# Performance work log

Measured on AMD Instinct MI355X. Metric: run time of the kernel, lower is better.

Reference implementation:

```python
import jax, jax.numpy as jnp
import numpy as np

B, T, C, E, K, CAP, H = 8, 2048, 1024, 8, 2, 4096, 4096


def setup_inputs() -> dict:
    key = jax.random.key(0)
    ks = jax.random.split(key, 6)
    s = 0.02
    return {
        "x": jax.random.normal(ks[0], (B, T, C), jnp.float32),
        "rw1": s * jax.random.normal(ks[1], (C, H), jnp.float32),
        "rb1": jnp.zeros((H,), jnp.float32),
        "rw2": s * jax.random.normal(ks[2], (H, E), jnp.float32),
        "rb2": jnp.zeros((E,), jnp.float32),
        "ew1": s * jax.random.normal(ks[3], (E, C, H), jnp.float32),
        "eb1": jnp.zeros((E, H), jnp.float32),
        "ew2": s * jax.random.normal(ks[4], (E, H, C), jnp.float32),
        "eb2": jnp.zeros((E, C), jnp.float32),
    }


def reference(x, rw1, rb1, rw2, rb2, ew1, eb1, ew2, eb2):
    Bx, Tx, Cx = x.shape
    N = Bx * Tx
    # Router FFN -> gating logits [B,T,E]
    logits = jax.nn.relu(x @ rw1 + rb1) @ rw2 + rb2
    vals, ids = jax.lax.top_k(logits, K)           # [B,T,K]
    probs = jax.nn.softmax(vals, axis=-1)          # [B,T,K]

    ids_f = ids.reshape(N * K)                     # expert id per (token, k) slot
    probs_f = probs.reshape(N * K)
    xr = jnp.repeat(x.reshape(N, Cx), K, axis=0)   # [N*K, C], token order preserved

    # position of each slot within its expert's capacity buffer
    m = jax.nn.one_hot(ids_f, E, dtype=jnp.int32)  # [N*K, E]
    pos = jnp.cumsum(m, axis=0) - 1
    pos_tok = jnp.take_along_axis(pos, ids_f[:, None], axis=1)[:, 0]
    keep = (pos_tok < CAP).astype(x.dtype)         # drop tokens over capacity (padding)
    pos_c = jnp.clip(pos_tok, 0, CAP - 1)

    # dispatch: scatter tokens into per-expert padded buffers [E, CAP, C]
    disp = jnp.zeros((E, CAP, Cx), x.dtype).at[ids_f, pos_c].add(xr * keep[:, None])

    # expert FFN, batched over experts
    h = jax.nn.relu(jnp.einsum('enc,ech->enh', disp, ew1) + eb1[:, None, :])
    eo = jnp.einsum('enh,ehc->enc', h, ew2) + eb2[:, None, :]

    # combine: gather expert outputs back, weight by gate prob, sum over k
    y = eo[ids_f, pos_c] * (probs_f * keep)[:, None]   # [N*K, C]
    return y.reshape(Bx, Tx, K, Cx).sum(axis=2)
```

## Files before the change

kernel.cpp:

```cpp
#include <hip/hip_runtime.h>
#include <cstdint>
#include <type_traits>

#define B_    8
#define T_    2048
#define C_    1024
#define E_    8
#define K_    2
#define CAP_  4096
#define H_    4096
#define NTOK  (B_ * T_)
#define NSLOT (NTOK * K_)
#define KR_   3072
#define MARGIN_ 8e-3f

typedef __bf16    bf16x8 __attribute__((ext_vector_type(8)));
typedef _Float16  half8  __attribute__((ext_vector_type(8)));
typedef float     f32x4  __attribute__((ext_vector_type(4)));

#define AS1 __attribute__((address_space(1)))
#define AS3 __attribute__((address_space(3)))

static __device__ __forceinline__ float b2f(unsigned short u) {
    union { float f; unsigned int i; } v; v.i = ((unsigned int)u) << 16; return v.f;
}
static __device__ __forceinline__ unsigned short f2b(float f) {
    unsigned int x = __float_as_uint(f);
    unsigned int r = (x + 0x7fffu + ((x >> 16) & 1u)) >> 16;
    return (unsigned short)r;
}
static __device__ __forceinline__ unsigned short f2h(float f) {
    _Float16 h = (_Float16)f;
    return __builtin_bit_cast(unsigned short, h);
}

template<int W> static __device__ __forceinline__ void vm_wait() {
    if constexpr (W == 4) asm volatile("s_waitcnt vmcnt(4)" ::: "memory");
    else if constexpr (W == 0) asm volatile("s_waitcnt vmcnt(0)" ::: "memory");
}

template<int RELU, typename TC, bool F16, bool SCAT>
__global__ __launch_bounds__(512, 2) void gemm256_8ph(
    const unsigned short* __restrict__ A, const unsigned short* __restrict__ BT,
    const float* __restrict__ bias, TC* __restrict__ Cout,
    int Kd, int Nld, int NT,
    long sA, long sB, long sBias, long sC,
    const int* __restrict__ lst, const int* __restrict__ cnt)
{
    extern __shared__ char smem[];

    const int z = blockIdx.z;
    A    += (size_t)z * sA;
    BT   += (size_t)z * sB;
    bias += (size_t)z * sBias;
    Cout += (size_t)z * sC;

    const int gx = gridDim.x;
    const int nwg = gx * gridDim.y;
    int wg = blockIdx.y * gx + blockIdx.x;
    wg = (wg & 7) * (nwg >> 3) + (wg >> 3);
    const int bm = (wg / gx) * 256;
    const int bn = (wg % gx) * 256;

    int nf = 0;
    if constexpr (SCAT) {
        nf = *cnt;
        if (bm >= nf) return;
    }

    const int tid  = threadIdx.x;
    const int lane = tid & 63;
    const int wid  = tid >> 6;
    const int wrow = (wid >> 2) * 128;
    const int wcol = (wid & 3) * 64;
    const int fr = lane & 15;
    const int fq = lane >> 4;

    const size_t rbA = (size_t)Kd * 2;
    const char* Ag = (const char*)A  + (size_t)bm * rbA;
    const char* Bg = (const char*)BT + (size_t)bn * rbA;

    f32x4 acc[8][4];
#pragma unroll
    for (int i = 0; i < 8; i++)
#pragma unroll
        for (int j = 0; j < 4; j++) acc[i][j] = (f32x4){0.f, 0.f, 0.f, 0.f};

    auto STAGE_A = [&](int kt) {
        char* d = smem + (size_t)(kt & 1) * 65536;
        const size_t kb = (size_t)kt * 128;
#pragma unroll
        for (int r = 0; r < 4; ++r) {
            const int o    = r * 8192 + tid * 16;
            const int row  = o >> 7;
            const int slot = (o >> 4) & 7;
            const int ss   = (slot ^ (row & 7)) << 4;
            __builtin_amdgcn_global_load_lds(
                (const AS1 void*)(Ag + (size_t)row * rbA + kb + ss),
                (AS3 void*)(d + r * 8192 + wid * 1024), 16, 0, 0);
        }
    };
    auto STAGE_B = [&](int kt) {
        char* d = smem + (size_t)(kt & 1) * 65536 + 32768;
        const size_t kb = (size_t)kt * 128;
#pragma unroll
        for (int r = 0; r < 4; ++r) {
            const int o    = r * 8192 + tid * 16;
            const int row  = o >> 7;
            const int slot = (o >> 4) & 7;
            const int ss   = (slot ^ (row & 7)) << 4;
            __builtin_amdgcn_global_load_lds(
                (const AS1 void*)(Bg + (size_t)row * rbA + kb + ss),
                (AS3 void*)(d + r * 8192 + wid * 1024), 16, 0, 0);
        }
    };

    auto LDA = [&](int kt, int mi, int kk) -> bf16x8 {
        const char* base = smem + (size_t)(kt & 1) * 65536;
        const int row  = wrow + mi * 16 + fr;
        const int slot = (kk * 4 + fq) ^ (row & 7);
        return *(const bf16x8*)(base + row * 128 + slot * 16);
    };
    auto LDB = [&](int kt, int ni, int kk) -> bf16x8 {
        const char* base = smem + (size_t)(kt & 1) * 65536 + 32768;
        const int row  = wcol + ni * 16 + fr;
        const int slot = (kk * 4 + fq) ^ (row & 7);
        return *(const bf16x8*)(base + row * 128 + slot * 16);
    };
    auto MFMA = [&](f32x4 c, bf16x8 a, bf16x8 b) -> f32x4 {
        if constexpr (F16)
            return __builtin_amdgcn_mfma_f32_16x16x32_f16(
                __builtin_bit_cast(half8, a), __builtin_bit_cast(half8, b), c, 0, 0, 0);
        else
            return __builtin_amdgcn_mfma_f32_16x16x32_bf16(a, b, c, 0, 0, 0);
    };

    STAGE_A(0); STAGE_B(0); STAGE_B(1);
    vm_wait<4>();
    __builtin_amdgcn_s_barrier();

    bf16x8 a[4], bb[4];
    for (int kt = 0; kt < NT; ++kt) {
#pragma unroll
        for (int i = 0; i < 4; ++i) a[i]  = LDA(kt, i, 0);
#pragma unroll
        for (int i = 0; i < 4; ++i) bb[i] = LDB(kt, i, 0);
        if (kt + 1 < NT) STAGE_A(kt + 1);
        __builtin_amdgcn_s_barrier();
        __builtin_amdgcn_s_setprio(1);
#pragma unroll
        for (int mi = 0; mi < 4; ++mi)
#pragma unroll
            for (int ni = 0; ni < 4; ++ni)
                acc[mi][ni] = MFMA(acc[mi][ni], a[mi], bb[ni]);
        __builtin_amdgcn_s_setprio(0);
        __builtin_amdgcn_s_barrier();
#pragma unroll
        for (int i = 0; i < 4; ++i) a[i] = LDA(kt, 4 + i, 0);
        __builtin_amdgcn_s_barrier();
        __builtin_amdgcn_s_setprio(1);
#pragma unroll
        for (int mi = 0; mi < 4; ++mi)
#pragma unroll
            for (int ni = 0; ni < 4; ++ni)
                acc[4 + mi][ni] = MFMA(acc[4 + mi][ni], a[mi], bb[ni]);
        __builtin_amdgcn_s_setprio(0);
        __builtin_amdgcn_s_barrier();
#pragma unroll
        for (int i = 0; i < 4; ++i) a[i]  = LDA(kt, i, 1);
#pragma unroll
        for (int i = 0; i < 4; ++i) bb[i] = LDB(kt, i, 1);
        __builtin_amdgcn_s_barrier();
        __builtin_amdgcn_s_setprio(1);
#pragma unroll
        for (int mi = 0; mi < 4; ++mi)
#pragma unroll
            for (int ni = 0; ni < 4; ++ni)
                acc[mi][ni] = MFMA(acc[mi][ni], a[mi], bb[ni]);
        __builtin_amdgcn_s_setprio(0);
        __builtin_amdgcn_s_barrier();
#pragma unroll
        for (int i = 0; i < 4; ++i) a[i] = LDA(kt, 4 + i, 1);
        if (kt + 2 < NT) STAGE_B(kt + 2);
        if (kt + 1 < NT) {
            if (kt + 2 < NT) vm_wait<4>();
            else             vm_wait<0>();
        }
        __builtin_amdgcn_s_barrier();
        __builtin_amdgcn_s_setprio(1);
#pragma unroll
        for (int mi = 0; mi < 4; ++mi)
#pragma unroll
            for (int ni = 0; ni < 4; ++ni)
                acc[4 + mi][ni] = MFMA(acc[4 + mi][ni], a[mi], bb[ni]);
        __builtin_amdgcn_s_setprio(0);
        __builtin_amdgcn_s_barrier();
    }

    const float* bias_o = bias;
    asm volatile("" : "+s"(bias_o));
#pragma unroll
    for (int mi = 0; mi < 8; ++mi) {
#pragma unroll
        for (int ni = 0; ni < 4; ++ni) {
            const int c = bn + wcol + ni * 16 + fr;
            const float bv = bias_o[c];
#pragma unroll
            for (int rg = 0; rg < 4; ++rg) {
                const int r = bm + wrow + mi * 16 + fq * 4 + rg;
                float v = acc[mi][ni][rg] + bv;
                if (RELU) v = fmaxf(v, 0.f);
                if constexpr (SCAT) {
                    if (r < nf) {
                        const int t = lst[r];
                        ((float*)Cout)[(size_t)t * Nld + c] = v;
                    }
                } else if constexpr (std::is_same_v<TC, float>) {
                    Cout[(size_t)r * Nld + c] = v;
                } else {
                    Cout[(size_t)r * Nld + c] = f2b(v);
                }
            }
        }
    }
}

__global__ __launch_bounds__(256) void split_x16(
    const float* __restrict__ x, unsigned short* __restrict__ x16)
{
    const int n = blockIdx.x;
    const int c = threadIdx.x * 4;
    const float4 v = *(const float4*)(x + (size_t)n * C_ + c);
    ushort4 u;
    u.x = f2h(v.x); u.y = f2h(v.y); u.z = f2h(v.z); u.w = f2h(v.w);
    *(ushort4*)(x16 + (size_t)n * C_ + c) = u;
}

__global__ __launch_bounds__(256) void gather_split(
    const float* __restrict__ x, const int* __restrict__ list,
    const int* __restrict__ count, unsigned short* __restrict__ Axc)
{
    const int i = blockIdx.x;
    if (i >= *count) return;
    const int n = list[i];
    const int c = threadIdx.x * 4;
    const float4 v = *(const float4*)(x + (size_t)n * C_ + c);
    ushort4 hi, lo;
    hi.x = f2b(v.x); lo.x = f2b(v.x - b2f(hi.x));
    hi.y = f2b(v.y); lo.y = f2b(v.y - b2f(hi.y));
    hi.z = f2b(v.z); lo.z = f2b(v.z - b2f(hi.z));
    hi.w = f2b(v.w); lo.w = f2b(v.w - b2f(hi.w));
    unsigned short* row = Axc + (size_t)i * KR_;
    *(ushort4*)(row + c)          = hi;
    *(ushort4*)(row + C_ + c)     = lo;
    *(ushort4*)(row + 2 * C_ + c) = hi;
}

__global__ __launch_bounds__(256) void split_w(
    const float* __restrict__ in, unsigned short* __restrict__ out)
{
    __shared__ float t[32][33];
    const int rb = blockIdx.y * 32;
    const int cb = blockIdx.x * 32;
    const int tr = threadIdx.x >> 3, tc = (threadIdx.x & 7) * 4;
    const float4 v = *(const float4*)(in + (size_t)(rb + tr) * H_ + cb + tc);
    t[tr][tc + 0] = v.x; t[tr][tc + 1] = v.y; t[tr][tc + 2] = v.z; t[tr][tc + 3] = v.w;
    __syncthreads();
    ushort4 hi, lo;
    float f;
    f = t[tc + 0][tr]; hi.x = f2b(f); lo.x = f2b(f - b2f(hi.x));
    f = t[tc + 1][tr]; hi.y = f2b(f); lo.y = f2b(f - b2f(hi.y));
    f = t[tc + 2][tr]; hi.z = f2b(f); lo.z = f2b(f - b2f(hi.z));
    f = t[tc + 3][tr]; hi.w = f2b(f); lo.w = f2b(f - b2f(hi.w));
    unsigned short* row = out + (size_t)(cb + tr) * KR_;
    *(ushort4*)(row + rb + tc)           = hi;
    *(ushort4*)(row + C_ + rb + tc)      = hi;
    *(ushort4*)(row + 2 * C_ + rb + tc)  = lo;
}

template<bool H16>
__global__ __launch_bounds__(256) void transpose_cvt(
    const float* __restrict__ in, unsigned short* __restrict__ out, int R, int Ncols)
{
    __shared__ float t[32][33];
    const size_t zoff = (size_t)blockIdx.z * R * Ncols;
    in  += zoff;
    out += zoff;
    const int rb = blockIdx.y * 32, cb = blockIdx.x * 32;
    const int tr = threadIdx.x >> 3, tc = (threadIdx.x & 7) * 4;
    const float4 v = *(const float4*)(in + (size_t)(rb + tr) * Ncols + cb + tc);
    t[tr][tc + 0] = v.x; t[tr][tc + 1] = v.y; t[tr][tc + 2] = v.z; t[tr][tc + 3] = v.w;
    __syncthreads();
    ushort4 u;
    if constexpr (H16) {
        u.x = f2h(t[tc + 0][tr]); u.y = f2h(t[tc + 1][tr]);
        u.z = f2h(t[tc + 2][tr]); u.w = f2h(t[tc + 3][tr]);
    } else {
        u.x = f2b(t[tc + 0][tr]); u.y = f2b(t[tc + 1][tr]);
        u.z = f2b(t[tc + 2][tr]); u.w = f2b(t[tc + 3][tr]);
    }
    *(ushort4*)(out + (size_t)(cb + tr) * R + rb + tc) = u;
}

template<int MODE>
__global__ __launch_bounds__(256) void router_topk_m(
    const float* __restrict__ h1, const float* __restrict__ rw2,
    const float* __restrict__ rb2, int* __restrict__ ids, float* __restrict__ probs,
    int* __restrict__ flagv, int* __restrict__ list, int* __restrict__ count)
{
    const int n = blockIdx.x;
    if (MODE == 1 && !flagv[n]) return;
    const float* hrow = h1 + (size_t)n * H_;
    float acc[E_];
#pragma unroll
    for (int e = 0; e < E_; e++) acc[e] = 0.f;
    for (int h = threadIdx.x; h < H_; h += 256) {
        const float hv = hrow[h];
        const float4 w0 = *(const float4*)(rw2 + (size_t)h * E_);
        const float4 w1 = *(const float4*)(rw2 + (size_t)h * E_ + 4);
        acc[0] = fmaf(hv, w0.x, acc[0]); acc[1] = fmaf(hv, w0.y, acc[1]);
        acc[2] = fmaf(hv, w0.z, acc[2]); acc[3] = fmaf(hv, w0.w, acc[3]);
        acc[4] = fmaf(hv, w1.x, acc[4]); acc[5] = fmaf(hv, w1.y, acc[5]);
        acc[6] = fmaf(hv, w1.z, acc[6]); acc[7] = fmaf(hv, w1.w, acc[7]);
    }
    __shared__ float red[E_][256];
#pragma unroll
    for (int e = 0; e < E_; e++) red[e][threadIdx.x] = acc[e];
    __syncthreads();
    for (int st = 128; st > 0; st >>= 1) {
        if (threadIdx.x < st) {
#pragma unroll
            for (int e = 0; e < E_; e++) red[e][threadIdx.x] += red[e][threadIdx.x + st];
        }
        __syncthreads();
    }
    if (threadIdx.x == 0) {
        float v1 = -1e30f, v2 = -1e30f, v3 = -1e30f; int i1 = 0, i2 = 0;
#pragma unroll
        for (int e = 0; e < E_; e++) {
            const float v = red[e][0] + rb2[e];
            if (v > v1)      { v3 = v2; v2 = v1; i2 = i1; v1 = v; i1 = e; }
            else if (v > v2) { v3 = v2; v2 = v;  i2 = e; }
            else if (v > v3) { v3 = v; }
        }
        const float e2 = expf(v2 - v1);
        const float inv = 1.f / (1.f + e2);
        ids[n * 2] = i1;  ids[n * 2 + 1] = i2;
        probs[n * 2] = inv; probs[n * 2 + 1] = e2 * inv;
        if (MODE == 0) {
            if ((v1 - v2 < MARGIN_) || (v2 - v3 < MARGIN_)) {
                flagv[n] = 1;
                const int idx = atomicAdd(count, 1);
                list[idx] = n;
            }
        }
    }
}

__global__ __launch_bounds__(256) void compute_pos(
    const int* __restrict__ ids, int* __restrict__ pos)
{
    __shared__ int hist[256][E_];
    const int t = threadIdx.x;
    const int per = NSLOT / 256;
    int cnt[E_];
#pragma unroll
    for (int e = 0; e < E_; e++) cnt[e] = 0;
    const int s0 = t * per;
    for (int i = 0; i < per; i++) cnt[ids[s0 + i]]++;
#pragma unroll
    for (int e = 0; e < E_; e++) hist[t][e] = cnt[e];
    __syncthreads();
    if (t < E_) {
        int run = 0;
        for (int i = 0; i < 256; i++) { const int c = hist[i][t]; hist[i][t] = run; run += c; }
    }
    __syncthreads();
    int run[E_];
#pragma unroll
    for (int e = 0; e < E_; e++) run[e] = hist[t][e];
    for (int i = 0; i < per; i++) { const int e = ids[s0 + i]; pos[s0 + i] = run[e]++; }
}

__global__ __launch_bounds__(256) void dispatch_k(
    const float* __restrict__ x, const int* __restrict__ ids,
    const int* __restrict__ pos, unsigned short* __restrict__ disp)
{
    const int s = blockIdx.x;
    const int e = ids[s], p = pos[s];
    if (p >= CAP_) return;
    const int n = s >> 1;
    const float4 v = *(const float4*)(x + (size_t)n * C_ + threadIdx.x * 4);
    ushort4 u;
    u.x = f2b(v.x); u.y = f2b(v.y); u.z = f2b(v.z); u.w = f2b(v.w);
    *(ushort4*)(disp + ((size_t)e * CAP_ + p) * C_ + threadIdx.x * 4) = u;
}

__global__ __launch_bounds__(256) void combine_k(
    const unsigned short* __restrict__ eo, const int* __restrict__ ids,
    const int* __restrict__ pos, const float* __restrict__ probs,
    float* __restrict__ y)
{
    const int n = blockIdx.x;
    const int c = threadIdx.x * 4;
    float r0 = 0.f, r1 = 0.f, r2 = 0.f, r3 = 0.f;
#pragma unroll
    for (int k = 0; k < K_; k++) {
        const int p = pos[2 * n + k];
        if (p >= CAP_) continue;
        const int e = ids[2 * n + k];
        const float w = probs[2 * n + k];
        const ushort4 u = *(const ushort4*)(eo + ((size_t)e * CAP_ + p) * C_ + c);
        r0 = fmaf(w, b2f(u.x), r0); r1 = fmaf(w, b2f(u.y), r1);
        r2 = fmaf(w, b2f(u.z), r2); r3 = fmaf(w, b2f(u.w), r3);
    }
    *(float4*)(y + (size_t)n * C_ + c) = make_float4(r0, r1, r2, r3);
}

extern "C" void kernel_launch(void* const* d_in, const int* in_sizes, int n_in,
                              void* d_out, int out_size, void* d_ws, size_t ws_size,
                              hipStream_t stream)
{
    const float* x   = (const float*)d_in[0];
    const float* rw1 = (const float*)d_in[1];
    const float* rb1 = (const float*)d_in[2];
    const float* rw2 = (const float*)d_in[3];
    const float* rb2 = (const float*)d_in[4];
    const float* ew1 = (const float*)d_in[5];
    const float* eb1 = (const float*)d_in[6];
    const float* ew2 = (const float*)d_in[7];
    const float* eb2 = (const float*)d_in[8];
    float* y = (float*)d_out;

    char* ws = (char*)d_ws;
    float*          h1    = (float*)ws;
    unsigned short* hexp  = (unsigned short*)ws;
    unsigned short* W16T  = (unsigned short*)(ws + 268435456L);
    unsigned short* Axc   = (unsigned short*)(ws + 268435456L);
    unsigned short* disp  = (unsigned short*)(ws + 268435456L);
    unsigned short* eo    = (unsigned short*)(ws + 268435456L);
    unsigned short* BTW   = (unsigned short*)(ws + 335544320L);
    unsigned short* B2    = (unsigned short*)(ws + 369098752L);
    unsigned short* x16   = (unsigned short*)(ws + 369098752L);
    int*            ids   = (int*)  (ws + 402653184L);
    float*          probs = (float*)(ws + 402784256L);
    int*            pos   = (int*)  (ws + 402915328L);
    int*            flagv = (int*)  (ws + 403046400L);
    int*            list  = (int*)  (ws + 403111936L);
    int*            count = (int*)  (ws + 403177472L);

    const size_t LDSB = 131072;

    hipMemsetAsync(count, 0, 128, stream);
    hipMemsetAsync(flagv, 0, NTOK * sizeof(int), stream);

    split_x16<<<NTOK, 256, 0, stream>>>(x, x16);
    {
        dim3 g(H_ / 32, C_ / 32, 1);
        transpose_cvt<true><<<g, 256, 0, stream>>>(rw1, W16T, C_, H_);
    }
    {
        dim3 g(H_ / 256, NTOK / 256, 1);
        gemm256_8ph<1, float, true, false><<<g, 512, LDSB, stream>>>(
            x16, W16T, rb1, h1, C_, H_, C_ / 64, 0, 0, 0, 0, nullptr, nullptr);
    }
    router_topk_m<0><<<NTOK, 256, 0, stream>>>(h1, rw2, rb2, ids, probs,
                                               flagv, list, count);
    gather_split<<<NTOK, 256, 0, stream>>>(x, list, count, Axc);
    {
        dim3 g(H_ / 32, C_ / 32, 1);
        split_w<<<g, 256, 0, stream>>>(rw1, B2);
    }
    {
        dim3 g(H_ / 256, NTOK / 256, 1);
        gemm256_8ph<1, float, false, true><<<g, 512, LDSB, stream>>>(
            Axc, B2, rb1, h1, KR_, H_, KR_ / 64, 0, 0, 0, 0, list, count);
    }
    router_topk_m<1><<<NTOK, 256, 0, stream>>>(h1, rw2, rb2, ids, probs,
                                               flagv, list, count);
    compute_pos<<<1, 256, 0, stream>>>(ids, pos);
    dispatch_k<<<NSLOT, 256, 0, stream>>>(x, ids, pos, disp);
    {
        dim3 g(H_ / 32, C_ / 32, E_);
        transpose_cvt<false><<<g, 256, 0, stream>>>(ew1, BTW, C_, H_);
    }
    {
        dim3 g(H_ / 256, CAP_ / 256, E_);
        gemm256_8ph<1, unsigned short, false, false><<<g, 512, LDSB, stream>>>(
            disp, BTW, eb1, hexp, C_, H_, C_ / 64,
            (long)CAP_ * C_, (long)H_ * C_, (long)H_, (long)CAP_ * H_,
            nullptr, nullptr);
    }
    {
        dim3 g(C_ / 32, H_ / 32, E_);
        transpose_cvt<false><<<g, 256, 0, stream>>>(ew2, BTW, H_, C_);
    }
    {
        dim3 g(C_ / 256, CAP_ / 256, E_);
        gemm256_8ph<0, unsigned short, false, false><<<g, 512, LDSB, stream>>>(
            hexp, BTW, eb2, eo, H_, C_, H_ / 64,
            (long)CAP_ * H_, (long)C_ * H_, (long)C_, (long)CAP_ * C_,
            nullptr, nullptr);
    }
    combine_k<<<NTOK, 256, 0, stream>>>(eo, ids, pos, probs, y);
}
```

Before: 1.208 ms.

## Store router hidden in bf16, fix flagged tokens densely, fuse combine into expert GEMM

The first router GEMM now writes its hidden activations as bf16 instead of fp32, and the top-k kernel reads that bf16 buffer. The near-tie margin is widened so more tokens are recomputed in higher precision; their hidden rows go to a compact buffer indexed by list position instead of being scattered. The separate combine kernel is removed. The second expert GEMM epilogue now atomically adds prob-weighted outputs into y through a slot_of map, which y and slot_of memsets set up. This saves the h1 fp32 traffic and the eo round trip, but adds atomics, a larger fix-up set, and order-dependent float sums.

```diff
diff --git a/kernel.cpp b/kernel.cpp
--- a/kernel.cpp
+++ b/kernel.cpp
@@ -12,7 +12,8 @@
 #define NTOK  (B_ * T_)
 #define NSLOT (NTOK * K_)
 #define KR_   3072
-#define MARGIN_ 8e-3f
+#define MARGIN_ 3e-2f
+#define FIXCAP 8192
 
 typedef __bf16    bf16x8 __attribute__((ext_vector_type(8)));
 typedef _Float16  half8  __attribute__((ext_vector_type(8)));
@@ -39,13 +40,14 @@
     else if constexpr (W == 0) asm volatile("s_waitcnt vmcnt(0)" ::: "memory");
 }
 
-template<int RELU, typename TC, bool F16, bool SCAT>
+template<int RELU, typename TC, bool F16, int EPI>
 __global__ __launch_bounds__(512, 2) void gemm256_8ph(
     const unsigned short* __restrict__ A, const unsigned short* __restrict__ BT,
     const float* __restrict__ bias, TC* __restrict__ Cout,
     int Kd, int Nld, int NT,
     long sA, long sB, long sBias, long sC,
-    const int* __restrict__ lst, const int* __restrict__ cnt)
+    const int* __restrict__ cnt, const int* __restrict__ slotof,
+    const float* __restrict__ probsv, float* __restrict__ yout)
 {
     extern __shared__ char smem[];
 
@@ -63,7 +65,7 @@
     const int bn = (wg % gx) * 256;
 
     int nf = 0;
-    if constexpr (SCAT) {
+    if constexpr (EPI == 1) {
         nf = *cnt;
         if (bm >= nf) return;
     }
@@ -210,11 +212,13 @@
                 const int r = bm + wrow + mi * 16 + fq * 4 + rg;
                 float v = acc[mi][ni][rg] + bv;
                 if (RELU) v = fmaxf(v, 0.f);
-                if constexpr (SCAT) {
-                    if (r < nf) {
-                        const int t = lst[r];
-                        ((float*)Cout)[(size_t)t * Nld + c] = v;
-                    }
+                if constexpr (EPI == 1) {
+                    if (r < nf)
+                        ((float*)Cout)[(size_t)r * Nld + c] = v;
+                } else if constexpr (EPI == 2) {
+                    const int s = slotof[z * CAP_ + r];
+                    if (s >= 0)
+                        atomicAdd(yout + (size_t)(s >> 1) * Nld + c, v * probsv[s]);
                 } else if constexpr (std::is_same_v<TC, float>) {
                     Cout[(size_t)r * Nld + c] = v;
                 } else {
@@ -302,26 +306,32 @@
     *(ushort4*)(out + (size_t)(cb + tr) * R + rb + tc) = u;
 }
 
-template<int MODE>
-__global__ __launch_bounds__(256) void router_topk_m(
-    const float* __restrict__ h1, const float* __restrict__ rw2,
+__global__ __launch_bounds__(256) void router_topk_approx(
+    const unsigned short* __restrict__ h1, const float* __restrict__ rw2,
     const float* __restrict__ rb2, int* __restrict__ ids, float* __restrict__ probs,
-    int* __restrict__ flagv, int* __restrict__ list, int* __restrict__ count)
+    int* __restrict__ iofn, int* __restrict__ list, int* __restrict__ count)
 {
     const int n = blockIdx.x;
-    if (MODE == 1 && !flagv[n]) return;
-    const float* hrow = h1 + (size_t)n * H_;
+    const unsigned short* hrow = h1 + (size_t)n * H_;
     float acc[E_];
 #pragma unroll
     for (int e = 0; e < E_; e++) acc[e] = 0.f;
-    for (int h = threadIdx.x; h < H_; h += 256) {
-        const float hv = hrow[h];
-        const float4 w0 = *(const float4*)(rw2 + (size_t)h * E_);
-        const float4 w1 = *(const float4*)(rw2 + (size_t)h * E_ + 4);
-        acc[0] = fmaf(hv, w0.x, acc[0]); acc[1] = fmaf(hv, w0.y, acc[1]);
-        acc[2] = fmaf(hv, w0.z, acc[2]); acc[3] = fmaf(hv, w0.w, acc[3]);
-        acc[4] = fmaf(hv, w1.x, acc[4]); acc[5] = fmaf(hv, w1.y, acc[5]);
-        acc[6] = fmaf(hv, w1.z, acc[6]); acc[7] = fmaf(hv, w1.w, acc[7]);
+    const int i0 = threadIdx.x * 16;
+#pragma unroll
+    for (int c4 = 0; c4 < 16; c4 += 4) {
+        const ushort4 u = *(const ushort4*)(hrow + i0 + c4);
+        const float hv0 = b2f(u.x), hv1 = b2f(u.y), hv2 = b2f(u.z), hv3 = b2f(u.w);
+        const float hvv[4] = {hv0, hv1, hv2, hv3};
+#pragma unroll
+        for (int k = 0; k < 4; ++k) {
+            const float hv = hvv[k];
+            const float4 w0 = *(const float4*)(rw2 + (size_t)(i0 + c4 + k) * E_);
+            const float4 w1 = *(const float4*)(rw2 + (size_t)(i0 + c4 + k) * E_ + 4);
+            acc[0] = fmaf(hv, w0.x, acc[0]); acc[1] = fmaf(hv, w0.y, acc[1]);
+            acc[2] = fmaf(hv, w0.z, acc[2]); acc[3] = fmaf(hv, w0.w, acc[3]);
+            acc[4] = fmaf(hv, w1.x, acc[4]); acc[5] = fmaf(hv, w1.y, acc[5]);
+            acc[6] = fmaf(hv, w1.z, acc[6]); acc[7] = fmaf(hv, w1.w, acc[7]);
+        }
     }
     __shared__ float red[E_][256];
 #pragma unroll
@@ -347,13 +357,66 @@
         const float inv = 1.f / (1.f + e2);
         ids[n * 2] = i1;  ids[n * 2 + 1] = i2;
         probs[n * 2] = inv; probs[n * 2 + 1] = e2 * inv;
-        if (MODE == 0) {
-            if ((v1 - v2 < MARGIN_) || (v2 - v3 < MARGIN_)) {
-                flagv[n] = 1;
-                const int idx = atomicAdd(count, 1);
-                list[idx] = n;
-            }
-        }
+        int idx = -1;
+        if ((v1 - v2 < MARGIN_) || (v2 - v3 < MARGIN_)) {
+            idx = atomicAdd(count, 1);
+            list[idx] = n;
+        }
+        iofn[n] = idx;
+    }
+}
+
+__global__ __launch_bounds__(256) void router_topk_fix(
+    const float* __restrict__ hfix, const float* __restrict__ rw2,
+    const float* __restrict__ rb2, int* __restrict__ ids, float* __restrict__ probs,
+    const int* __restrict__ iofn)
+{
+    const int n = blockIdx.x;
+    const int i = iofn[n];
+    if (i < 0) return;
+    const float* hrow = hfix + (size_t)i * H_;
+    float acc[E_];
+#pragma unroll
+    for (int e = 0; e < E_; e++) acc[e] = 0.f;
+    const int i0 = threadIdx.x * 16;
+#pragma unroll
+    for (int c4 = 0; c4 < 16; c4 += 4) {
+        const float4 h4 = *(const float4*)(hrow + i0 + c4);
+        const float hvv[4] = {h4.x, h4.y, h4.z, h4.w};
+#pragma unroll
+        for (int k = 0; k < 4; ++k) {
+            const float hv = hvv[k];
+            const float4 w0 = *(const float4*)(rw2 + (size_t)(i0 + c4 + k) * E_);
+            const float4 w1 = *(const float4*)(rw2 + (size_t)(i0 + c4 + k) * E_ + 4);
+            acc[0] = fmaf(hv, w0.x, acc[0]); acc[1] = fmaf(hv, w0.y, acc[1]);
+            acc[2] = fmaf(hv, w0.z, acc[2]); acc[3] = fmaf(hv, w0.w, acc[3]);
+            acc[4] = fmaf(hv, w1.x, acc[4]); acc[5] = fmaf(hv, w1.y, acc[5]);
+            acc[6] = fmaf(hv, w1.z, acc[6]); acc[7] = fmaf(hv, w1.w, acc[7]);
+        }
+    }
+    __shared__ float red[E_][256];
+#pragma unroll
+    for (int e = 0; e < E_; e++) red[e][threadIdx.x] = acc[e];
+    __syncthreads();
+    for (int st = 128; st > 0; st >>= 1) {
+        if (threadIdx.x < st) {
+#pragma unroll
+            for (int e = 0; e < E_; e++) red[e][threadIdx.x] += red[e][threadIdx.x + st];
+        }
+        __syncthreads();
+    }
+    if (threadIdx.x == 0) {
+        float v1 = -1e30f, v2 = -1e30f; int i1 = 0, i2 = 0;
+#pragma unroll
+        for (int e = 0; e < E_; e++) {
+            const float v = red[e][0] + rb2[e];
+            if (v > v1)      { v2 = v1; i2 = i1; v1 = v; i1 = e; }
+            else if (v > v2) { v2 = v;  i2 = e; }
+        }
+        const float e2 = expf(v2 - v1);
+        const float inv = 1.f / (1.f + e2);
+        ids[n * 2] = i1;  ids[n * 2 + 1] = i2;
+        probs[n * 2] = inv; probs[n * 2 + 1] = e2 * inv;
     }
 }
 
@@ -384,7 +447,8 @@
 
 __global__ __launch_bounds__(256) void dispatch_k(
     const float* __restrict__ x, const int* __restrict__ ids,
-    const int* __restrict__ pos, unsigned short* __restrict__ disp)
+    const int* __restrict__ pos, unsigned short* __restrict__ disp,
+    int* __restrict__ slot_of)
 {
     const int s = blockIdx.x;
     const int e = ids[s], p = pos[s];
@@ -394,27 +458,7 @@
     ushort4 u;
     u.x = f2b(v.x); u.y = f2b(v.y); u.z = f2b(v.z); u.w = f2b(v.w);
     *(ushort4*)(disp + ((size_t)e * CAP_ + p) * C_ + threadIdx.x * 4) = u;
-}
-
-__global__ __launch_bounds__(256) void combine_k(
-    const unsigned short* __restrict__ eo, const int* __restrict__ ids,
-    const int* __restrict__ pos, const float* __restrict__ probs,
-    float* __restrict__ y)
-{
-    const int n = blockIdx.x;
-    const int c = threadIdx.x * 4;
-    float r0 = 0.f, r1 = 0.f, r2 = 0.f, r3 = 0.f;
-#pragma unroll
-    for (int k = 0; k < K_; k++) {
-        const int p = pos[2 * n + k];
-        if (p >= CAP_) continue;
-        const int e = ids[2 * n + k];
-        const float w = probs[2 * n + k];
-        const ushort4 u = *(const ushort4*)(eo + ((size_t)e * CAP_ + p) * C_ + c);
-        r0 = fmaf(w, b2f(u.x), r0); r1 = fmaf(w, b2f(u.y), r1);
-        r2 = fmaf(w, b2f(u.z), r2); r3 = fmaf(w, b2f(u.w), r3);
-    }
-    *(float4*)(y + (size_t)n * C_ + c) = make_float4(r0, r1, r2, r3);
+    if (threadIdx.x == 0) slot_of[e * CAP_ + p] = s;
 }
 
 extern "C" void kernel_launch(void* const* d_in, const int* in_sizes, int n_in,
@@ -433,26 +477,28 @@
     float* y = (float*)d_out;
 
     char* ws = (char*)d_ws;
-    float*          h1    = (float*)ws;
-    unsigned short* hexp  = (unsigned short*)ws;
-    unsigned short* W16T  = (unsigned short*)(ws + 268435456L);
-    unsigned short* Axc   = (unsigned short*)(ws + 268435456L);
-    unsigned short* disp  = (unsigned short*)(ws + 268435456L);
-    unsigned short* eo    = (unsigned short*)(ws + 268435456L);
-    unsigned short* BTW   = (unsigned short*)(ws + 335544320L);
-    unsigned short* B2    = (unsigned short*)(ws + 369098752L);
-    unsigned short* x16   = (unsigned short*)(ws + 369098752L);
-    int*            ids   = (int*)  (ws + 402653184L);
-    float*          probs = (float*)(ws + 402784256L);
-    int*            pos   = (int*)  (ws + 402915328L);
-    int*            flagv = (int*)  (ws + 403046400L);
-    int*            list  = (int*)  (ws + 403111936L);
-    int*            count = (int*)  (ws + 403177472L);
+    unsigned short* h1b    = (unsigned short*)ws;
+    float*          hfix   = (float*)(ws + 134217728L);
+    unsigned short* hexp   = (unsigned short*)ws;
+    unsigned short* W16T   = (unsigned short*)(ws + 268435456L);
+    unsigned short* Axc    = (unsigned short*)(ws + 268435456L);
+    unsigned short* disp   = (unsigned short*)(ws + 268435456L);
+    unsigned short* BTW    = (unsigned short*)(ws + 335544320L);
+    unsigned short* B2     = (unsigned short*)(ws + 369098752L);
+    unsigned short* x16    = (unsigned short*)(ws + 369098752L);
+    int*            ids    = (int*)  (ws + 402653184L);
+    float*          probs  = (float*)(ws + 402784256L);
+    int*            pos    = (int*)  (ws + 402915328L);
+    int*            iofn   = (int*)  (ws + 403046400L);
+    int*            list   = (int*)  (ws + 403111936L);
+    int*            slot_of= (int*)  (ws + 403177472L);
+    int*            count  = (int*)  (ws + 403308544L);
 
     const size_t LDSB = 131072;
 
     hipMemsetAsync(count, 0, 128, stream);
-    hipMemsetAsync(flagv, 0, NTOK * sizeof(int), stream);
+    hipMemsetAsync(slot_of, 0xFF, (size_t)E_ * CAP_ * sizeof(int), stream);
+    hipMemsetAsync(y, 0, (size_t)out_size * sizeof(float), stream);
 
     split_x16<<<NTOK, 256, 0, stream>>>(x, x16);
     {
@@ -461,11 +507,12 @@
     }
     {
         dim3 g(H_ / 256, NTOK / 256, 1);
-        gemm256_8ph<1, float, true, false><<<g, 512, LDSB, stream>>>(
-            x16, W16T, rb1, h1, C_, H_, C_ / 64, 0, 0, 0, 0, nullptr, nullptr);
-    }
-    router_topk_m<0><<<NTOK, 256, 0, stream>>>(h1, rw2, rb2, ids, probs,
-                                               flagv, list, count);
+        gemm256_8ph<1, unsigned short, true, 0><<<g, 512, LDSB, stream>>>(
+            x16, W16T, rb1, h1b, C_, H_, C_ / 64, 0, 0, 0, 0,
+            nullptr, nullptr, nullptr, nullptr);
+    }
+    router_topk_approx<<<NTOK, 256, 0, stream>>>(h1b, rw2, rb2, ids, probs,
+                                                 iofn, list, count);
     gather_split<<<NTOK, 256, 0, stream>>>(x, list, count, Axc);
     {
         dim3 g(H_ / 32, C_ / 32, 1);
@@ -473,23 +520,23 @@
     }
     {
         dim3 g(H_ / 256, NTOK / 256, 1);
-        gemm256_8ph<1, float, false, true><<<g, 512, LDSB, stream>>>(
-            Axc, B2, rb1, h1, KR_, H_, KR_ / 64, 0, 0, 0, 0, list, count);
-    }
-    router_topk_m<1><<<NTOK, 256, 0, stream>>>(h1, rw2, rb2, ids, probs,
-                                               flagv, list, count);
+        gemm256_8ph<1, float, false, 1><<<g, 512, LDSB, stream>>>(
+            Axc, B2, rb1, hfix, KR_, H_, KR_ / 64, 0, 0, 0, 0,
+            count, nullptr, nullptr, nullptr);
+    }
+    router_topk_fix<<<NTOK, 256, 0, stream>>>(hfix, rw2, rb2, ids, probs, iofn);
     compute_pos<<<1, 256, 0, stream>>>(ids, pos);
-    dispatch_k<<<NSLOT, 256, 0, stream>>>(x, ids, pos, disp);
+    dispatch_k<<<NSLOT, 256, 0, stream>>>(x, ids, pos, disp, slot_of);
     {
         dim3 g(H_ / 32, C_ / 32, E_);
         transpose_cvt<false><<<g, 256, 0, stream>>>(ew1, BTW, C_, H_);
     }
     {
         dim3 g(H_ / 256, CAP_ / 256, E_);
-        gemm256_8ph<1, unsigned short, false, false><<<g, 512, LDSB, stream>>>(
+        gemm256_8ph<1, unsigned short, false, 0><<<g, 512, LDSB, stream>>>(
             disp, BTW, eb1, hexp, C_, H_, C_ / 64,
             (long)CAP_ * C_, (long)H_ * C_, (long)H_, (long)CAP_ * H_,
-            nullptr, nullptr);
+            nullptr, nullptr, nullptr, nullptr);
     }
     {
         dim3 g(C_ / 32, H_ / 32, E_);
@@ -497,10 +544,9 @@
     }
     {
         dim3 g(C_ / 256, CAP_ / 256, E_);
-        gemm256_8ph<0, unsigned short, false, false><<<g, 512, LDSB, stream>>>(
-            hexp, BTW, eb2, eo, H_, C_, H_ / 64,
-            (long)CAP_ * H_, (long)C_ * H_, (long)C_, (long)CAP_ * C_,
-            nullptr, nullptr);
-    }
-    combine_k<<<NTOK, 256, 0, stream>>>(eo, ids, pos, probs, y);
-}
+        gemm256_8ph<0, float, false, 2><<<g, 512, LDSB, stream>>>(
+            hexp, BTW, eb2, y, H_, C_, H_ / 64,
+            (long)CAP_ * H_, (long)C_ * H_, (long)C_, 0,
+            nullptr, slot_of, probs, y);
+    }
+}
```

New measurement: 1.690 ms. 1.4x slower.

## Fuse router second layer into first router GEMM epilogue, compact refinement buffer

Applied to the files above, without the earlier changes.

The first router GEMM no longer writes the full fp32 hidden activations (16384x4096). Instead its epilogue applies ReLU, multiplies by rw2 and reduces partial logits per 256-column tile through LDS into a small buffer. A new per-token kernel sums those partials, does top-2 and flags near-tie tokens. The refinement GEMM now writes a compact buffer indexed by list position, capped at a fixed count. This removes a large write and read of the hidden activations, but adds register and LDS pressure to the epilogue, and any flagged tokens beyond the cap keep their fp16 routing.

```diff
diff --git a/kernel.cpp b/kernel.cpp
--- a/kernel.cpp
+++ b/kernel.cpp
@@ -13,6 +13,7 @@
 #define NSLOT (NTOK * K_)
 #define KR_   3072
 #define MARGIN_ 8e-3f
+#define FIXCAP 4096
 
 typedef __bf16    bf16x8 __attribute__((ext_vector_type(8)));
 typedef _Float16  half8  __attribute__((ext_vector_type(8)));
@@ -39,13 +40,14 @@
     else if constexpr (W == 0) asm volatile("s_waitcnt vmcnt(0)" ::: "memory");
 }
 
-template<int RELU, typename TC, bool F16, bool SCAT>
+template<int RELU, typename TC, bool F16, int EPI>
 __global__ __launch_bounds__(512, 2) void gemm256_8ph(
     const unsigned short* __restrict__ A, const unsigned short* __restrict__ BT,
     const float* __restrict__ bias, TC* __restrict__ Cout,
     int Kd, int Nld, int NT,
     long sA, long sB, long sBias, long sC,
-    const int* __restrict__ lst, const int* __restrict__ cnt)
+    const int* __restrict__ cnt,
+    const float* __restrict__ rw2v, float* __restrict__ plogv)
 {
     extern __shared__ char smem[];
 
@@ -53,7 +55,7 @@
     A    += (size_t)z * sA;
     BT   += (size_t)z * sB;
     bias += (size_t)z * sBias;
-    Cout += (size_t)z * sC;
+    if constexpr (EPI == 0) Cout += (size_t)z * sC;
 
     const int gx = gridDim.x;
     const int nwg = gx * gridDim.y;
@@ -63,8 +65,9 @@
     const int bn = (wg % gx) * 256;
 
     int nf = 0;
-    if constexpr (SCAT) {
+    if constexpr (EPI == 1) {
         nf = *cnt;
+        if (nf > FIXCAP) nf = FIXCAP;
         if (bm >= nf) return;
     }
 
@@ -127,12 +130,12 @@
         const int slot = (kk * 4 + fq) ^ (row & 7);
         return *(const bf16x8*)(base + row * 128 + slot * 16);
     };
-    auto MFMA = [&](f32x4 c, bf16x8 a, bf16x8 b) -> f32x4 {
+    auto MFMA = [&](f32x4 c, bf16x8 av, bf16x8 bv) -> f32x4 {
         if constexpr (F16)
             return __builtin_amdgcn_mfma_f32_16x16x32_f16(
-                __builtin_bit_cast(half8, a), __builtin_bit_cast(half8, b), c, 0, 0, 0);
+                __builtin_bit_cast(half8, av), __builtin_bit_cast(half8, bv), c, 0, 0, 0);
         else
-            return __builtin_amdgcn_mfma_f32_16x16x32_bf16(a, b, c, 0, 0, 0);
+            return __builtin_amdgcn_mfma_f32_16x16x32_bf16(av, bv, c, 0, 0, 0);
     };
 
     STAGE_A(0); STAGE_B(0); STAGE_B(1);
@@ -199,29 +202,180 @@
 
     const float* bias_o = bias;
     asm volatile("" : "+s"(bias_o));
-#pragma unroll
-    for (int mi = 0; mi < 8; ++mi) {
+
+    if constexpr (EPI == 3) {
+        float w2r[4][8];
 #pragma unroll
         for (int ni = 0; ni < 4; ++ni) {
-            const int c = bn + wcol + ni * 16 + fr;
-            const float bv = bias_o[c];
+            const float* src = rw2v + (size_t)(bn + wcol + ni * 16 + fr) * 8;
+            *(float4*)(w2r[ni])     = *(const float4*)(src);
+            *(float4*)(w2r[ni] + 4) = *(const float4*)(src + 4);
+        }
+        float bv[4];
+#pragma unroll
+        for (int ni = 0; ni < 4; ++ni)
+            bv[ni] = bias_o[bn + wcol + ni * 16 + fr];
+
+        float* pb = (float*)smem;
+        const int rowhalf = wid >> 2, colwave = wid & 3;
+        const int frq = fr >> 2;
+
+#pragma unroll
+        for (int mi = 0; mi < 8; ++mi) {
 #pragma unroll
             for (int rg = 0; rg < 4; ++rg) {
-                const int r = bm + wrow + mi * 16 + fq * 4 + rg;
-                float v = acc[mi][ni][rg] + bv;
-                if (RELU) v = fmaxf(v, 0.f);
-                if constexpr (SCAT) {
-                    if (r < nf) {
-                        const int t = lst[r];
-                        ((float*)Cout)[(size_t)t * Nld + c] = v;
-                    }
-                } else if constexpr (std::is_same_v<TC, float>) {
-                    Cout[(size_t)r * Nld + c] = v;
-                } else {
-                    Cout[(size_t)r * Nld + c] = f2b(v);
+                float p[8];
+#pragma unroll
+                for (int e = 0; e < 8; ++e) p[e] = 0.f;
+#pragma unroll
+                for (int ni = 0; ni < 4; ++ni) {
+                    const float h = fmaxf(acc[mi][ni][rg] + bv[ni], 0.f);
+#pragma unroll
+                    for (int e = 0; e < 8; ++e) p[e] = fmaf(h, w2r[ni][e], p[e]);
+                }
+#pragma unroll
+                for (int e = 0; e < 8; ++e) {
+                    p[e] += __shfl_xor(p[e], 1);
+                    p[e] += __shfl_xor(p[e], 2);
+                }
+                if ((fr & 3) == 0) {
+                    const int row = mi * 16 + fq * 4 + rg;
+                    float* dst = pb +
+                        ((((size_t)rowhalf * 4 + colwave) * 128 + row) * 4 + frq) * 8;
+                    *(float4*)(dst)     = make_float4(p[0], p[1], p[2], p[3]);
+                    *(float4*)(dst + 4) = make_float4(p[4], p[5], p[6], p[7]);
                 }
             }
         }
+        __syncthreads();
+        {
+            const int r  = tid >> 1;
+            const int eh = (tid & 1) * 4;
+            const int rowhalf2 = r >> 7, rl = r & 127;
+            float4 s = make_float4(0.f, 0.f, 0.f, 0.f);
+#pragma unroll
+            for (int cw = 0; cw < 4; ++cw)
+#pragma unroll
+                for (int q = 0; q < 4; ++q) {
+                    const float4 v = *(const float4*)(pb +
+                        ((((size_t)rowhalf2 * 4 + cw) * 128 + rl) * 4 + q) * 8 + eh);
+                    s.x += v.x; s.y += v.y; s.z += v.z; s.w += v.w;
+                }
+            *(float4*)(plogv + ((size_t)(bn >> 8) * NTOK + bm + r) * 8 + eh) = s;
+        }
+    } else {
+#pragma unroll
+        for (int mi = 0; mi < 8; ++mi) {
+#pragma unroll
+            for (int ni = 0; ni < 4; ++ni) {
+                const int c = bn + wcol + ni * 16 + fr;
+                const float bv = bias_o[c];
+#pragma unroll
+                for (int rg = 0; rg < 4; ++rg) {
+                    const int r = bm + wrow + mi * 16 + fq * 4 + rg;
+                    float v = acc[mi][ni][rg] + bv;
+                    if (RELU) v = fmaxf(v, 0.f);
+                    if constexpr (EPI == 1) {
+                        if (r < nf)
+                            ((float*)Cout)[(size_t)r * Nld + c] = v;
+                    } else if constexpr (std::is_same_v<TC, float>) {
+                        Cout[(size_t)r * Nld + c] = v;
+                    } else {
+                        Cout[(size_t)r * Nld + c] = f2b(v);
+                    }
+                }
+            }
+        }
+    }
+}
+
+__global__ __launch_bounds__(256) void router_topk_flag(
+    const float* __restrict__ plog, const float* __restrict__ rb2,
+    int* __restrict__ ids, float* __restrict__ probs,
+    int* __restrict__ iofn, int* __restrict__ list, int* __restrict__ count)
+{
+    const int n = blockIdx.x * 256 + threadIdx.x;
+    float l[E_];
+#pragma unroll
+    for (int e = 0; e < E_; ++e) l[e] = rb2[e];
+#pragma unroll
+    for (int bx = 0; bx < 16; ++bx) {
+        const float4 a = *(const float4*)(plog + ((size_t)bx * NTOK + n) * 8);
+        const float4 b = *(const float4*)(plog + ((size_t)bx * NTOK + n) * 8 + 4);
+        l[0] += a.x; l[1] += a.y; l[2] += a.z; l[3] += a.w;
+        l[4] += b.x; l[5] += b.y; l[6] += b.z; l[7] += b.w;
+    }
+    float v1 = -1e30f, v2 = -1e30f, v3 = -1e30f; int i1 = 0, i2 = 0;
+#pragma unroll
+    for (int e = 0; e < E_; ++e) {
+        const float v = l[e];
+        if (v > v1)      { v3 = v2; v2 = v1; i2 = i1; v1 = v; i1 = e; }
+        else if (v > v2) { v3 = v2; v2 = v;  i2 = e; }
+        else if (v > v3) { v3 = v; }
+    }
+    const float e2 = expf(v2 - v1);
+    const float inv = 1.f / (1.f + e2);
+    ids[n * 2] = i1;  ids[n * 2 + 1] = i2;
+    probs[n * 2] = inv; probs[n * 2 + 1] = e2 * inv;
+    int idx = -1;
+    if ((v1 - v2 < MARGIN_) || (v2 - v3 < MARGIN_)) {
+        idx = atomicAdd(count, 1);
+        if (idx < FIXCAP) list[idx] = n; else idx = -1;
+    }
+    iofn[n] = idx;
+}
+
+__global__ __launch_bounds__(256) void router_topk_fix(
+    const float* __restrict__ hfix, const float* __restrict__ rw2,
+    const float* __restrict__ rb2, int* __restrict__ ids, float* __restrict__ probs,
+    const int* __restrict__ iofn)
+{
+    const int n = blockIdx.x;
+    const int i = iofn[n];
+    if (i < 0) return;
+    const float* hrow = hfix + (size_t)i * H_;
+    float acc[E_];
+#pragma unroll
+    for (int e = 0; e < E_; e++) acc[e] = 0.f;
+    const int i0 = threadIdx.x * 16;
+#pragma unroll
+    for (int c4 = 0; c4 < 16; c4 += 4) {
+        const float4 h4 = *(const float4*)(hrow + i0 + c4);
+        const float hvv[4] = {h4.x, h4.y, h4.z, h4.w};
+#pragma unroll
+        for (int k = 0; k < 4; ++k) {
+            const float hv = hvv[k];
+            const float4 w0 = *(const float4*)(rw2 + (size_t)(i0 + c4 + k) * E_);
+            const float4 w1 = *(const float4*)(rw2 + (size_t)(i0 + c4 + k) * E_ + 4);
+            acc[0] = fmaf(hv, w0.x, acc[0]); acc[1] = fmaf(hv, w0.y, acc[1]);
+            acc[2] = fmaf(hv, w0.z, acc[2]); acc[3] = fmaf(hv, w0.w, acc[3]);
+            acc[4] = fmaf(hv, w1.x, acc[4]); acc[5] = fmaf(hv, w1.y, acc[5]);
+            acc[6] = fmaf(hv, w1.z, acc[6]); acc[7] = fmaf(hv, w1.w, acc[7]);
+        }
+    }
+    __shared__ float red[E_][256];
+#pragma unroll
+    for (int e = 0; e < E_; e++) red[e][threadIdx.x] = acc[e];
+    __syncthreads();
+    for (int st = 128; st > 0; st >>= 1) {
+        if (threadIdx.x < st) {
+#pragma unroll
+            for (int e = 0; e < E_; e++) red[e][threadIdx.x] += red[e][threadIdx.x + st];
+        }
+        __syncthreads();
+    }
+    if (threadIdx.x == 0) {
+        float v1 = -1e30f, v2 = -1e30f; int i1 = 0, i2 = 0;
+#pragma unroll
+        for (int e = 0; e < E_; e++) {
+            const float v = red[e][0] + rb2[e];
+            if (v > v1)      { v2 = v1; i2 = i1; v1 = v; i1 = e; }
+            else if (v > v2) { v2 = v;  i2 = e; }
+        }
+        const float e2 = expf(v2 - v1);
+        const float inv = 1.f / (1.f + e2);
+        ids[n * 2] = i1;  ids[n * 2 + 1] = i2;
+        probs[n * 2] = inv; probs[n * 2 + 1] = e2 * inv;
     }
 }
 
@@ -241,7 +395,8 @@
     const int* __restrict__ count, unsigned short* __restrict__ Axc)
 {
     const int i = blockIdx.x;
-    if (i >= *count) return;
+    int nf = *count; if (nf > FIXCAP) nf = FIXCAP;
+    if (i >= nf) return;
     const int n = list[i];
     const int c = threadIdx.x * 4;
     const float4 v = *(const float4*)(x + (size_t)n * C_ + c);
@@ -302,61 +457,6 @@
     *(ushort4*)(out + (size_t)(cb + tr) * R + rb + tc) = u;
 }
 
-template<int MODE>
-__global__ __launch_bounds__(256) void router_topk_m(
-    const float* __restrict__ h1, const float* __restrict__ rw2,
-    const float* __restrict__ rb2, int* __restrict__ ids, float* __restrict__ probs,
-    int* __restrict__ flagv, int* __restrict__ list, int* __restrict__ count)
-{
-    const int n = blockIdx.x;
-    if (MODE == 1 && !flagv[n]) return;
-    const float* hrow = h1 + (size_t)n * H_;
-    float acc[E_];
-#pragma unroll
-    for (int e = 0; e < E_; e++) acc[e] = 0.f;
-    for (int h = threadIdx.x; h < H_; h += 256) {
-        const float hv = hrow[h];
-        const float4 w0 = *(const float4*)(rw2 + (size_t)h * E_);
-        const float4 w1 = *(const float4*)(rw2 + (size_t)h * E_ + 4);
-        acc[0] = fmaf(hv, w0.x, acc[0]); acc[1] = fmaf(hv, w0.y, acc[1]);
-        acc[2] = fmaf(hv, w0.z, acc[2]); acc[3] = fmaf(hv, w0.w, acc[3]);
-        acc[4] = fmaf(hv, w1.x, acc[4]); acc[5] = fmaf(hv, w1.y, acc[5]);
-        acc[6] = fmaf(hv, w1.z, acc[6]); acc[7] = fmaf(hv, w1.w, acc[7]);
-    }
-    __shared__ float red[E_][256];
-#pragma unroll
-    for (int e = 0; e < E_; e++) red[e][threadIdx.x] = acc[e];
-    __syncthreads();
-    for (int st = 128; st > 0; st >>= 1) {
-        if (threadIdx.x < st) {
-#pragma unroll
-            for (int e = 0; e < E_; e++) red[e][threadIdx.x] += red[e][threadIdx.x + st];
-        }
-        __syncthreads();
-    }
-    if (threadIdx.x == 0) {
-        float v1 = -1e30f, v2 = -1e30f, v3 = -1e30f; int i1 = 0, i2 = 0;
-#pragma unroll
-        for (int e = 0; e < E_; e++) {
-            const float v = red[e][0] + rb2[e];
-            if (v > v1)      { v3 = v2; v2 = v1; i2 = i1; v1 = v; i1 = e; }
-            else if (v > v2) { v3 = v2; v2 = v;  i2 = e; }
-            else if (v > v3) { v3 = v; }
-        }
-        const float e2 = expf(v2 - v1);
-        const float inv = 1.f / (1.f + e2);
-        ids[n * 2] = i1;  ids[n * 2 + 1] = i2;
-        probs[n * 2] = inv; probs[n * 2 + 1] = e2 * inv;
-        if (MODE == 0) {
-            if ((v1 - v2 < MARGIN_) || (v2 - v3 < MARGIN_)) {
-                flagv[n] = 1;
-                const int idx = atomicAdd(count, 1);
-                list[idx] = n;
-            }
-        }
-    }
-}
-
 __global__ __launch_bounds__(256) void compute_pos(
     const int* __restrict__ ids, int* __restrict__ pos)
 {
@@ -433,51 +533,49 @@
     float* y = (float*)d_out;
 
     char* ws = (char*)d_ws;
-    float*          h1    = (float*)ws;
     unsigned short* hexp  = (unsigned short*)ws;
-    unsigned short* W16T  = (unsigned short*)(ws + 268435456L);
+    unsigned short* x16   = (unsigned short*)(ws + 268435456L);
     unsigned short* Axc   = (unsigned short*)(ws + 268435456L);
     unsigned short* disp  = (unsigned short*)(ws + 268435456L);
     unsigned short* eo    = (unsigned short*)(ws + 268435456L);
+    unsigned short* W16T  = (unsigned short*)(ws + 301989888L);
+    unsigned short* B2    = (unsigned short*)(ws + 310378496L);
+    float*          hfix  = (float*)(ws + 335544320L);
     unsigned short* BTW   = (unsigned short*)(ws + 335544320L);
-    unsigned short* B2    = (unsigned short*)(ws + 369098752L);
-    unsigned short* x16   = (unsigned short*)(ws + 369098752L);
+    float*          plog  = (float*)(ws + 394264576L);
     int*            ids   = (int*)  (ws + 402653184L);
     float*          probs = (float*)(ws + 402784256L);
     int*            pos   = (int*)  (ws + 402915328L);
-    int*            flagv = (int*)  (ws + 403046400L);
+    int*            iofn  = (int*)  (ws + 403046400L);
     int*            list  = (int*)  (ws + 403111936L);
     int*            count = (int*)  (ws + 403177472L);
 
     const size_t LDSB = 131072;
 
     hipMemsetAsync(count, 0, 128, stream);
-    hipMemsetAsync(flagv, 0, NTOK * sizeof(int), stream);
 
     split_x16<<<NTOK, 256, 0, stream>>>(x, x16);
     {
         dim3 g(H_ / 32, C_ / 32, 1);
         transpose_cvt<true><<<g, 256, 0, stream>>>(rw1, W16T, C_, H_);
+        split_w<<<g, 256, 0, stream>>>(rw1, B2);
     }
     {
         dim3 g(H_ / 256, NTOK / 256, 1);
-        gemm256_8ph<1, float, true, false><<<g, 512, LDSB, stream>>>(
-            x16, W16T, rb1, h1, C_, H_, C_ / 64, 0, 0, 0, 0, nullptr, nullptr);
-    }
-    router_topk_m<0><<<NTOK, 256, 0, stream>>>(h1, rw2, rb2, ids, probs,
-                                               flagv, list, count);
+        gemm256_8ph<1, float, true, 3><<<g, 512, LDSB, stream>>>(
+            x16, W16T, rb1, (float*)nullptr, C_, H_, C_ / 64, 0, 0, 0, 0,
+            nullptr, rw2, plog);
+    }
+    router_topk_flag<<<NTOK / 256, 256, 0, stream>>>(plog, rb2, ids, probs,
+                                                     iofn, list, count);
     gather_split<<<NTOK, 256, 0, stream>>>(x, list, count, Axc);
     {
-        dim3 g(H_ / 32, C_ / 32, 1);
-        split_w<<<g, 256, 0, stream>>>(rw1, B2);
-    }
-    {
         dim3 g(H_ / 256, NTOK / 256, 1);
-        gemm256_8ph<1, float, false, true><<<g, 512, LDSB, stream>>>(
-            Axc, B2, rb1, h1, KR_, H_, KR_ / 64, 0, 0, 0, 0, list, count);
-    }
-    router_topk_m<1><<<NTOK, 256, 0, stream>>>(h1, rw2, rb2, ids, probs,
-                                               flagv, list, count);
+        gemm256_8ph<1, float, false, 1><<<g, 512, LDSB, stream>>>(
+            Axc, B2, rb1, hfix, KR_, H_, KR_ / 64, 0, 0, 0, 0,
+            count, nullptr, nullptr);
+    }
+    router_topk_fix<<<NTOK, 256, 0, stream>>>(hfix, rw2, rb2, ids, probs, iofn);
     compute_pos<<<1, 256, 0, stream>>>(ids, pos);
     dispatch_k<<<NSLOT, 256, 0, stream>>>(x, ids, pos, disp);
     {
@@ -486,10 +584,10 @@
     }
     {
         dim3 g(H_ / 256, CAP_ / 256, E_);
-        gemm256_8ph<1, unsigned short, false, false><<<g, 512, LDSB, stream>>>(
+        gemm256_8ph<1, unsigned short, false, 0><<<g, 512, LDSB, stream>>>(
             disp, BTW, eb1, hexp, C_, H_, C_ / 64,
             (long)CAP_ * C_, (long)H_ * C_, (long)H_, (long)CAP_ * H_,
-            nullptr, nullptr);
+            nullptr, nullptr, nullptr);
     }
     {
         dim3 g(C_ / 32, H_ / 32, E_);
@@ -497,10 +595,10 @@
     }
     {
         dim3 g(C_ / 256, CAP_ / 256, E_);
-        gemm256_8ph<0, unsigned short, false, false><<<g, 512, LDSB, stream>>>(
+        gemm256_8ph<0, unsigned short, false, 0><<<g, 512, LDSB, stream>>>(
             hexp, BTW, eb2, eo, H_, C_, H_ / 64,
             (long)CAP_ * H_, (long)C_ * H_, (long)C_, (long)CAP_ * C_,
-            nullptr, nullptr);
+            nullptr, nullptr, nullptr);
     }
     combine_k<<<NTOK, 256, 0, stream>>>(eo, ids, pos, probs, y);
 }
```

New measurement: 1.094 ms. 1.1x faster.
